# Kernel tuning notes

Measured on AMD Instinct MI355X. Metric: run time of the kernel, lower is better.

The kernel has to match this reference:

```python
import jax, jax.numpy as jnp
import numpy as np

D = 1024
H = 16
HD = D // H
DFF = 4 * D
EPS = 1e-12


def setup_inputs() -> dict:
    key = jax.random.key(0)
    ks = jax.random.split(key, 16)
    s = lambda fan_in: 1.0 / np.sqrt(fan_in)
    inp = {
        "x": jax.random.normal(ks[0], (2, 2048, D), dtype=jnp.float32),
        "Wq": jax.random.normal(ks[1], (D, D), dtype=jnp.float32) * s(D),
        "bq": jax.random.normal(ks[2], (D,), dtype=jnp.float32) * 0.02,
        "Wk": jax.random.normal(ks[3], (D, D), dtype=jnp.float32) * s(D),
        "bk": jax.random.normal(ks[4], (D,), dtype=jnp.float32) * 0.02,
        "Wv": jax.random.normal(ks[5], (D, D), dtype=jnp.float32) * s(D),
        "bv": jax.random.normal(ks[6], (D,), dtype=jnp.float32) * 0.02,
        "Wo": jax.random.normal(ks[7], (D, D), dtype=jnp.float32) * s(D),
        "bo": jax.random.normal(ks[8], (D,), dtype=jnp.float32) * 0.02,
        "W1": jax.random.normal(ks[9], (D, DFF), dtype=jnp.float32) * s(D),
        "b1": jax.random.normal(ks[10], (DFF,), dtype=jnp.float32) * 0.02,
        "W2": jax.random.normal(ks[11], (DFF, D), dtype=jnp.float32) * s(DFF),
        "b2": jax.random.normal(ks[12], (D,), dtype=jnp.float32) * 0.02,
        "g1": jnp.ones((D,), dtype=jnp.float32),
        "s1": jnp.zeros((D,), dtype=jnp.float32),
        "g2": jnp.ones((D,), dtype=jnp.float32),
        "s2": jnp.zeros((D,), dtype=jnp.float32),
    }
    return inp


def _layer_norm(x, scale, shift):
    mean = jnp.mean(x, axis=-1, keepdims=True)
    # torch.var default is unbiased (ddof=1), matching the source module
    var = jnp.var(x, axis=-1, keepdims=True, ddof=1)
    return scale * (x - mean) / jnp.sqrt(var + EPS) + shift


def _gelu(x):
    c = jnp.sqrt(jnp.asarray(2.0 / np.pi, dtype=x.dtype))
    return 0.5 * x * (1.0 + jnp.tanh(c * (x + 0.044715 * x ** 3)))


def _block(x, Wq, bq, Wk, bk, Wv, bv, Wo, bo, W1, b1, W2, b2, g1, s1, g2, s2):
    B, S, _ = x.shape
    # pre-norm attention
    h = _layer_norm(x, g1, s1)
    q = (h @ Wq + bq).reshape(B, S, H, HD).transpose(0, 2, 1, 3)  # bhsd
    k = (h @ Wk + bk).reshape(B, S, H, HD).transpose(0, 2, 1, 3)
    v = (h @ Wv + bv).reshape(B, S, H, HD).transpose(0, 2, 1, 3)
    scores = jnp.einsum("bhqd,bhkd->bhqk", q, k)
    causal = jnp.tril(jnp.ones((S, S), dtype=bool))  # True = keep
    scores = jnp.where(causal, scores, -jnp.inf)
    attn = jax.nn.softmax(scores / np.sqrt(HD), axis=-1)
    ctx = jnp.einsum("bhqk,bhkd->bhqd", attn, v)
    ctx = ctx.transpose(0, 2, 1, 3).reshape(B, S, D)
    x = x + (ctx @ Wo + bo)
    # pre-norm MLP
    h = _layer_norm(x, g2, s2)
    h = _gelu(h @ W1 + b1) @ W2 + b2
    return x + h


def reference(x, Wq, bq, Wk, bk, Wv, bv, Wo, bo, W1, b1, W2, b2, g1, s1, g2, s2):
    return _block(x, Wq, bq, Wk, bk, Wv, bv, Wo, bo, W1, b1, W2, b2, g1, s1, g2, s2)
```

## Files before the change

kernel.cpp:

```cpp
#include <hip/hip_runtime.h>

#define D_ 1024
#define H_ 16
#define HD_ 64
#define DFF_ 4096
#define B_ 2
#define S_ 2048
#define MTOK 4096

typedef unsigned short u16;
typedef short bf16x8 __attribute__((ext_vector_type(8)));
typedef float f32x4 __attribute__((ext_vector_type(4)));

__device__ __forceinline__ u16 f2bf(float f) {
    union { float f; unsigned u; } v; v.f = f;
    return (u16)((v.u + 0x7fffu + ((v.u >> 16) & 1u)) >> 16);
}
__device__ __forceinline__ u16 f2bf_ru(float f) {
    union { float f; unsigned u; } v; v.f = f;
    return (u16)((v.u + 0x8000u) >> 16);
}

__device__ __forceinline__ void gload16(const void* g, void* l) {
    __builtin_amdgcn_global_load_lds(
        (const __attribute__((address_space(1))) unsigned int*)g,
        (__attribute__((address_space(3))) unsigned int*)l, 16, 0, 0);
}

__global__ __launch_bounds__(256) void transpose_cast_kernel(
    const float* __restrict__ W, u16* __restrict__ Wt, int K, int N) {
    __shared__ float t[32][33];
    int n0 = blockIdx.x * 32, k0 = blockIdx.y * 32;
    int tx = threadIdx.x, ty = threadIdx.y;
#pragma unroll
    for (int i = 0; i < 4; i++)
        t[ty + i * 8][tx] = W[(size_t)(k0 + ty + i * 8) * N + n0 + tx];
    __syncthreads();
#pragma unroll
    for (int i = 0; i < 4; i++)
        Wt[(size_t)(n0 + ty + i * 8) * K + k0 + tx] = f2bf(t[tx][ty + i * 8]);
}

__global__ __launch_bounds__(256) void ln_kernel(
    const float* __restrict__ x, const float* __restrict__ gamma,
    const float* __restrict__ beta, u16* __restrict__ out) {
    int row = blockIdx.x, tid = threadIdx.x;
    int wave = tid >> 6, lane = tid & 63;
    const float4* xr = (const float4*)(x + (size_t)row * D_);
    float4 v = xr[tid];
    float s = v.x + v.y + v.z + v.w;
#pragma unroll
    for (int off = 1; off < 64; off <<= 1) s += __shfl_xor(s, off, 64);
    __shared__ float p1[4], p2[4];
    if (lane == 0) p1[wave] = s;
    __syncthreads();
    float mean = (p1[0] + p1[1] + p1[2] + p1[3]) * (1.0f / D_);
    float4 d = {v.x - mean, v.y - mean, v.z - mean, v.w - mean};
    float sq = d.x * d.x + d.y * d.y + d.z * d.z + d.w * d.w;
#pragma unroll
    for (int off = 1; off < 64; off <<= 1) sq += __shfl_xor(sq, off, 64);
    if (lane == 0) p2[wave] = sq;
    __syncthreads();
    float var = (p2[0] + p2[1] + p2[2] + p2[3]) * (1.0f / (D_ - 1));
    float rstd = rsqrtf(var + 1e-12f);
    float4 gv = ((const float4*)gamma)[tid];
    float4 bv = ((const float4*)beta)[tid];
    u16* orow = out + (size_t)row * D_ + tid * 4;
    orow[0] = f2bf(gv.x * d.x * rstd + bv.x);
    orow[1] = f2bf(gv.y * d.y * rstd + bv.y);
    orow[2] = f2bf(gv.z * d.z * rstd + bv.z);
    orow[3] = f2bf(gv.w * d.w * rstd + bv.w);
}

constexpr int EPI_QKV = 0, EPI_O = 3, EPI_G = 4, EPI_R = 5;

template <int EPI, int KD, int TM, int BK, int GYB>
__global__ __launch_bounds__(256) void gemm_kernel(
    const u16* __restrict__ A, const u16* __restrict__ Bt,
    const float* __restrict__ bias, const float* __restrict__ bias2,
    const float* __restrict__ bias3, const float* __restrict__ resid,
    void* __restrict__ Cout) {
    __shared__ alignas(16) char Alds[2][TM * BK * 2];
    __shared__ alignas(16) char Blds[2][128 * BK * 2];
    int tid = threadIdx.x;
    int tm = (blockIdx.x & ((1 << GYB) - 1)) * TM;
    int tn = (blockIdx.x >> GYB) * 128;
    int wave = tid >> 6, lane = tid & 63;
    int wrow = (wave >> 1) * (TM / 2), wcol = (wave & 1) * 64;
    int lcol = lane & 15, quad = lane >> 4;
    constexpr int NI = TM / 32;
    f32x4 acc[NI][4] = {};

    const u16 *ga, *gb;
    if constexpr (BK == 32) {
        int l = lane >> 3, p = lane & 7, slog = p ^ l;
        int sro = l * 2 + (slog >> 2), sch = slog & 3;
        ga = A + (size_t)(tm + wave * 16 + sro) * KD + sch * 8;
        gb = Bt + (size_t)(tn + wave * 16 + sro) * KD + sch * 8;
    } else {
        int g = (lane & 7) ^ (lane >> 3);
        ga = A + (size_t)(tm + wave * 16 + (lane >> 3)) * KD + g * 8;
        gb = Bt + (size_t)(tn + wave * 32 + (lane >> 3)) * KD + g * 8;
    }

    auto stage = [&](int k0, int buf) {
        if constexpr (BK == 32) {
            char* lA = Alds[buf] + wave * 1024;
            char* lB = Blds[buf] + wave * 1024;
            gload16(ga + k0, lA);
            if constexpr (TM == 128) gload16(ga + (size_t)64 * KD + k0, lA + 4096);
            gload16(gb + k0, lB);
            gload16(gb + (size_t)64 * KD + k0, lB + 4096);
        } else {
            char* lA = Alds[buf] + wave * 2048;
            gload16(ga + k0, lA);
            gload16(ga + (size_t)8 * KD + k0, lA + 1024);
            char* lB = Blds[buf] + wave * 4096;
            gload16(gb + k0, lB);
            gload16(gb + (size_t)8 * KD + k0, lB + 1024);
            gload16(gb + (size_t)16 * KD + k0, lB + 2048);
            gload16(gb + (size_t)24 * KD + k0, lB + 3072);
        }
    };

    constexpr int NT = KD / BK;
    stage(0, 0);
    int cur = 0;
#pragma unroll 1
    for (int kt = 0; kt < NT; kt++) {
        __syncthreads();
        if (kt + 1 < NT) stage((kt + 1) * BK, cur ^ 1);
        if constexpr (BK == 32) {
            int swz = (lcol >> 1) * 128 + (((((lcol & 1) << 2) | quad) ^ (lcol >> 1)) * 16);
            bf16x8 af[NI], bfr[4];
#pragma unroll
            for (int i = 0; i < NI; i++)
                af[i] = *(const bf16x8*)(Alds[cur] + wrow * 64 + i * 1024 + swz);
#pragma unroll
            for (int j = 0; j < 4; j++)
                bfr[j] = *(const bf16x8*)(Blds[cur] + wcol * 64 + j * 1024 + swz);
#pragma unroll
            for (int i = 0; i < NI; i++)
#pragma unroll
                for (int j = 0; j < 4; j++)
                    acc[i][j] = __builtin_amdgcn_mfma_f32_16x16x32_bf16(
                        af[i], bfr[j], acc[i][j], 0, 0, 0);
        } else {
            int koff0 = lcol * 128 + ((quad ^ (lcol & 7)) * 16);
            int koff1 = lcol * 128 + (((4 | quad) ^ (lcol & 7)) * 16);
            bf16x8 af0[NI], af1[NI], bf0[4], bf1[4];
#pragma unroll
            for (int i = 0; i < NI; i++) {
                af0[i] = *(const bf16x8*)(Alds[cur] + (wrow + i * 16) * 128 + koff0);
                af1[i] = *(const bf16x8*)(Alds[cur] + (wrow + i * 16) * 128 + koff1);
            }
#pragma unroll
            for (int j = 0; j < 4; j++) {
                bf0[j] = *(const bf16x8*)(Blds[cur] + (wcol + j * 16) * 128 + koff0);
                bf1[j] = *(const bf16x8*)(Blds[cur] + (wcol + j * 16) * 128 + koff1);
            }
#pragma unroll
            for (int i = 0; i < NI; i++)
#pragma unroll
                for (int j = 0; j < 4; j++)
                    acc[i][j] = __builtin_amdgcn_mfma_f32_16x16x32_bf16(
                        af0[i], bf0[j], acc[i][j], 0, 0, 0);
#pragma unroll
            for (int i = 0; i < NI; i++)
#pragma unroll
                for (int j = 0; j < 4; j++)
                    acc[i][j] = __builtin_amdgcn_mfma_f32_16x16x32_bf16(
                        af1[i], bf1[j], acc[i][j], 0, 0, 0);
        }
        cur ^= 1;
    }
#pragma unroll
    for (int i = 0; i < NI; i++)
#pragma unroll
        for (int j = 0; j < 4; j++)
#pragma unroll
            for (int r = 0; r < 4; r++) {
                int m = tm + wrow + i * 16 + quad * 4 + r;
                int n = tn + wcol + j * 16 + lcol;
                if constexpr (EPI == EPI_QKV) {
                    int which = n >> 10, d = n & 1023;
                    const float* bp = (which == 0) ? bias : (which == 1) ? bias2 : bias3;
                    float cval = acc[i][j][r] + bp[d];
                    int b = m >> 11, s = m & 2047, h = d >> 6, hd = d & 63;
                    u16* qkv = (u16*)Cout;
                    if (which == 0)
                        qkv[((size_t)(b * H_ + h) * S_ + s) * HD_ + hd] = f2bf(cval);
                    else if (which == 1)
                        qkv[4194304u + ((size_t)(b * H_ + h) * S_ + s) * HD_ + hd] = f2bf(cval);
                    else
                        qkv[8388608u + ((size_t)(b * H_ + h) * HD_ + hd) * S_ + s] = f2bf(cval);
                } else if constexpr (EPI == EPI_O) {
                    float cval = acc[i][j][r] + bias[n];
                    ((float*)Cout)[(size_t)m * D_ + n] = resid[(size_t)m * D_ + n] + cval;
                } else if constexpr (EPI == EPI_G) {
                    float cval = acc[i][j][r] + bias[n];
                    float u = 0.7978845608028654f * (cval + 0.044715f * cval * cval * cval);
                    float t = 1.0f - 2.0f / (__expf(2.0f * u) + 1.0f);
                    ((u16*)Cout)[(size_t)m * DFF_ + n] = f2bf(0.5f * cval * (1.0f + t));
                } else {
                    float cval = acc[i][j][r] + bias[n];
                    ((float*)Cout)[(size_t)m * D_ + n] = resid[(size_t)m * D_ + n] + cval;
                }
            }
}

__global__ __launch_bounds__(256) void attn_kernel(
    const u16* __restrict__ q, const u16* __restrict__ k,
    const u16* __restrict__ v, u16* __restrict__ ctx) {
    __shared__ alignas(16) u16 klds[2][64 * 64];
    __shared__ alignas(16) u16 vlds[2][64 * 64];
    __shared__ alignas(16) u16 plds[4][16 * 64];
    int tid = threadIdx.x, wave = tid >> 6, lane = tid & 63;
    int quad = lane >> 4, lcol = lane & 15;
    int bh = blockIdx.x & 31, pairi = blockIdx.x >> 5;
    const u16* qbase = q + (size_t)bh * S_ * HD_;
    const u16* kbase = k + (size_t)bh * S_ * HD_;
    const u16* vbase = v + (size_t)bh * HD_ * S_;
    int g = (lane & 7) ^ (lane >> 3);
    int srow = wave * 16 + (lane >> 3);
    const u16* kp = kbase + (size_t)srow * HD_ + g * 8;
    const u16* vp = vbase + (size_t)srow * S_ + g * 8;
    char* kd0 = (char*)klds[0] + wave * 2048;
    char* kd1 = (char*)klds[1] + wave * 2048;
    char* vd0 = (char*)vlds[0] + wave * 2048;
    char* vd1 = (char*)vlds[1] + wave * 2048;
    char* pbase = (char*)plds + wave * 2048;
    int koff0 = lcol * 128 + ((quad ^ (lcol & 7)) * 16);
    int koff1 = lcol * 128 + (((4 | quad) ^ (lcol & 7)) * 16);
    int b = bh >> 4, h = bh & 15;
#pragma unroll 1
    for (int half = 0; half < 2; half++) {
        int qt = half ? (31 - pairi) : pairi;
        int qr = qt * 64 + wave * 16;
        bf16x8 aq0 = *(const bf16x8*)(qbase + (size_t)(qr + lcol) * HD_ + quad * 8);
        bf16x8 aq1 = *(const bf16x8*)(qbase + (size_t)(qr + lcol) * HD_ + 32 + quad * 8);
        f32x4 co[4] = {};
        float li[4] = {0.0f, 0.0f, 0.0f, 0.0f};
        __syncthreads();
        gload16(kp, kd0);
        gload16(kp + (size_t)8 * HD_, kd0 + 1024);
        gload16(vp, vd0);
        gload16(vp + 8 * S_, vd0 + 1024);
        int cur = 0;
#pragma unroll 1
        for (int kt = 0; kt <= qt; kt++) {
            __syncthreads();
            if (kt < qt) {
                int k0 = (kt + 1) * 64;
                char* kd = cur ? kd0 : kd1;
                char* vd = cur ? vd0 : vd1;
                gload16(kp + (size_t)k0 * HD_, kd);
                gload16(kp + (size_t)(k0 + 8) * HD_, kd + 1024);
                gload16(vp + k0, vd);
                gload16(vp + 8 * S_ + k0, vd + 1024);
            }
            const u16* kl = klds[cur];
            const u16* vl = vlds[cur];
            f32x4 cs[4] = {};
#pragma unroll
            for (int j = 0; j < 4; j++) {
                bf16x8 bk = *(const bf16x8*)((char*)kl + j * 2048 + koff0);
                cs[j] = __builtin_amdgcn_mfma_f32_16x16x32_bf16(aq0, bk, cs[j], 0, 0, 0);
            }
#pragma unroll
            for (int j = 0; j < 4; j++) {
                bf16x8 bk = *(const bf16x8*)((char*)kl + j * 2048 + koff1);
                cs[j] = __builtin_amdgcn_mfma_f32_16x16x32_bf16(aq1, bk, cs[j], 0, 0, 0);
            }
            bool diag = (kt == qt);
#pragma unroll
            for (int r = 0; r < 4; r++) {
                int rr = quad * 4 + r;
                float p[4], ls = 0.0f;
#pragma unroll
                for (int j = 0; j < 4; j++) {
                    float sv = cs[j][r];
                    if (diag && (j * 16 + lcol > wave * 16 + rr)) sv = -1e38f;
                    p[j] = exp2f(sv * 0.18033688011112042f);
                    ls += p[j];
                }
                li[r] += ls;
                int pr = rr * 128 + (lcol & 7) * 2;
#pragma unroll
                for (int j = 0; j < 4; j++)
                    *(u16*)(pbase + pr + (((j * 2 + (lcol >> 3)) ^ (rr & 7)) * 16)) = f2bf_ru(p[j]);
            }
            {
                bf16x8 ap0 = *(const bf16x8*)(pbase + koff0);
                bf16x8 ap1 = *(const bf16x8*)(pbase + koff1);
#pragma unroll
                for (int j = 0; j < 4; j++) {
                    bf16x8 bv0 = *(const bf16x8*)((char*)vl + j * 2048 + koff0);
                    co[j] = __builtin_amdgcn_mfma_f32_16x16x32_bf16(ap0, bv0, co[j], 0, 0, 0);
                }
#pragma unroll
                for (int j = 0; j < 4; j++) {
                    bf16x8 bv1 = *(const bf16x8*)((char*)vl + j * 2048 + koff1);
                    co[j] = __builtin_amdgcn_mfma_f32_16x16x32_bf16(ap1, bv1, co[j], 0, 0, 0);
                }
            }
            cur ^= 1;
        }
#pragma unroll
        for (int r = 0; r < 4; r++) {
            float l = li[r];
            l += __shfl_xor(l, 1);
            l += __shfl_xor(l, 2);
            l += __shfl_xor(l, 4);
            l += __shfl_xor(l, 8);
            float inv = 1.0f / l;
            int row = qr + quad * 4 + r;
            size_t base = ((size_t)(b * S_ + row)) * D_ + h * HD_;
#pragma unroll
            for (int j = 0; j < 4; j++)
                ctx[base + j * 16 + lcol] = f2bf(co[j][r] * inv);
        }
    }
}

extern "C" void kernel_launch(void* const* d_in, const int* in_sizes, int n_in,
                              void* d_out, int out_size, void* d_ws, size_t ws_size,
                              hipStream_t stream) {
    const float* x  = (const float*)d_in[0];
    const float* Wq = (const float*)d_in[1];
    const float* bq = (const float*)d_in[2];
    const float* Wk = (const float*)d_in[3];
    const float* bk = (const float*)d_in[4];
    const float* Wv = (const float*)d_in[5];
    const float* bv = (const float*)d_in[6];
    const float* Wo = (const float*)d_in[7];
    const float* bo = (const float*)d_in[8];
    const float* W1 = (const float*)d_in[9];
    const float* b1 = (const float*)d_in[10];
    const float* W2 = (const float*)d_in[11];
    const float* b2 = (const float*)d_in[12];
    const float* g1 = (const float*)d_in[13];
    const float* s1 = (const float*)d_in[14];
    const float* g2 = (const float*)d_in[15];
    const float* s2 = (const float*)d_in[16];

    char* ws = (char*)d_ws;
    const size_t MB = 1024 * 1024;
    u16*   bWqkv = (u16*)(ws + 0 * MB);
    u16*   bWo   = (u16*)(ws + 6 * MB);
    u16*   bW1   = (u16*)(ws + 8 * MB);
    u16*   bW2   = (u16*)(ws + 16 * MB);
    u16*   hbuf  = (u16*)(ws + 24 * MB);
    u16*   qbuf  = (u16*)(ws + 32 * MB);
    u16*   ctxb  = (u16*)(ws + 56 * MB);
    float* x1    = (float*)(ws + 64 * MB);
    u16*   ffb   = (u16*)(ws + 80 * MB);

    dim3 tb(32, 8);
    transpose_cast_kernel<<<dim3(32, 32), tb, 0, stream>>>(Wq, bWqkv, D_, D_);
    transpose_cast_kernel<<<dim3(32, 32), tb, 0, stream>>>(Wk, bWqkv + 1024 * 1024, D_, D_);
    transpose_cast_kernel<<<dim3(32, 32), tb, 0, stream>>>(Wv, bWqkv + 2 * 1024 * 1024, D_, D_);
    transpose_cast_kernel<<<dim3(32, 32), tb, 0, stream>>>(Wo, bWo, D_, D_);
    transpose_cast_kernel<<<dim3(128, 32), tb, 0, stream>>>(W1, bW1, D_, DFF_);
    transpose_cast_kernel<<<dim3(32, 128), tb, 0, stream>>>(W2, bW2, DFF_, D_);

    ln_kernel<<<MTOK, 256, 0, stream>>>(x, g1, s1, hbuf);

    gemm_kernel<EPI_QKV, D_, 128, 32, 5><<<768, 256, 0, stream>>>(
        hbuf, bWqkv, bq, bk, bv, nullptr, qbuf);

    attn_kernel<<<512, 256, 0, stream>>>(
        qbuf, qbuf + 4194304u, qbuf + 8388608u, ctxb);

    gemm_kernel<EPI_O, D_, 64, 64, 6><<<512, 256, 0, stream>>>(
        ctxb, bWo, bo, nullptr, nullptr, x, x1);

    ln_kernel<<<MTOK, 256, 0, stream>>>(x1, g2, s2, hbuf);

    gemm_kernel<EPI_G, D_, 128, 32, 5><<<1024, 256, 0, stream>>>(
        hbuf, bW1, b1, nullptr, nullptr, nullptr, ffb);

    gemm_kernel<EPI_R, DFF_, 64, 64, 6><<<512, 256, 0, stream>>>(
        ffb, bW2, b2, nullptr, nullptr, x1, (float*)d_out);
}
```

Before: 357.9 us.

## Triple-buffer GEMM and attention loads and merge weight transposes into one launch

The GEMM and attention kernels move from double-buffered LDS staging with a full __syncthreads per tile to a three-slot ring that prefetches two tiles ahead. Each step waits with a partial s_waitcnt vmcnt followed by a raw s_barrier. The six weight transpose/cast launches are merged into one kernel that dispatches on block index, cutting launch overhead. The cost is 50% more LDS per block, which may lower occupancy, and the hand-set vmcnt values must match the exact number of loads issued per stage.

```diff
diff --git a/kernel.cpp b/kernel.cpp
--- a/kernel.cpp
+++ b/kernel.cpp
@@ -27,18 +27,38 @@
         (__attribute__((address_space(3))) unsigned int*)l, 16, 0, 0);
 }
 
-__global__ __launch_bounds__(256) void transpose_cast_kernel(
-    const float* __restrict__ W, u16* __restrict__ Wt, int K, int N) {
-    __shared__ float t[32][33];
-    int n0 = blockIdx.x * 32, k0 = blockIdx.y * 32;
+__global__ __launch_bounds__(256) void transpose_all_kernel(
+    const float* __restrict__ Wq, const float* __restrict__ Wk,
+    const float* __restrict__ Wv, const float* __restrict__ Wo,
+    const float* __restrict__ W1, const float* __restrict__ W2,
+    u16* __restrict__ bQKV, u16* __restrict__ bWo,
+    u16* __restrict__ bW1, u16* __restrict__ bW2) {
+    int b = blockIdx.x;
+    const float* W; u16* Wt; int K, N, nt, kt;
+    if (b < 4096) {
+        int w = b >> 10, t = b & 1023;
+        K = 1024; N = 1024; nt = t & 31; kt = t >> 5;
+        W = (w == 0) ? Wq : (w == 1) ? Wk : (w == 2) ? Wv : Wo;
+        Wt = (w < 3) ? (bQKV + (size_t)w * 1048576u) : bWo;
+    } else if (b < 8192) {
+        int t = b - 4096;
+        K = 1024; N = 4096; nt = t & 127; kt = t >> 7;
+        W = W1; Wt = bW1;
+    } else {
+        int t = b - 8192;
+        K = 4096; N = 1024; nt = t & 31; kt = t >> 5;
+        W = W2; Wt = bW2;
+    }
+    __shared__ float tl[32][33];
+    int n0 = nt * 32, k0 = kt * 32;
     int tx = threadIdx.x, ty = threadIdx.y;
 #pragma unroll
     for (int i = 0; i < 4; i++)
-        t[ty + i * 8][tx] = W[(size_t)(k0 + ty + i * 8) * N + n0 + tx];
+        tl[ty + i * 8][tx] = W[(size_t)(k0 + ty + i * 8) * N + n0 + tx];
     __syncthreads();
 #pragma unroll
     for (int i = 0; i < 4; i++)
-        Wt[(size_t)(n0 + ty + i * 8) * K + k0 + tx] = f2bf(t[tx][ty + i * 8]);
+        Wt[(size_t)(n0 + ty + i * 8) * K + k0 + tx] = f2bf(tl[tx][ty + i * 8]);
 }
 
 __global__ __launch_bounds__(256) void ln_kernel(
@@ -80,8 +100,8 @@
     const float* __restrict__ bias, const float* __restrict__ bias2,
     const float* __restrict__ bias3, const float* __restrict__ resid,
     void* __restrict__ Cout) {
-    __shared__ alignas(16) char Alds[2][TM * BK * 2];
-    __shared__ alignas(16) char Blds[2][128 * BK * 2];
+    __shared__ alignas(16) char Alds[3][TM * BK * 2];
+    __shared__ alignas(16) char Blds[3][128 * BK * 2];
     int tid = threadIdx.x;
     int tm = (blockIdx.x & ((1 << GYB) - 1)) * TM;
     int tn = (blockIdx.x >> GYB) * 128;
@@ -89,6 +109,7 @@
     int wrow = (wave >> 1) * (TM / 2), wcol = (wave & 1) * 64;
     int lcol = lane & 15, quad = lane >> 4;
     constexpr int NI = TM / 32;
+    constexpr int G = (BK == 32) ? 4 : 6;
     f32x4 acc[NI][4] = {};
 
     const u16 *ga, *gb;
@@ -103,19 +124,19 @@
         gb = Bt + (size_t)(tn + wave * 32 + (lane >> 3)) * KD + g * 8;
     }
 
-    auto stage = [&](int k0, int buf) {
+    auto stage = [&](int k0, int slot) {
         if constexpr (BK == 32) {
-            char* lA = Alds[buf] + wave * 1024;
-            char* lB = Blds[buf] + wave * 1024;
+            char* lA = Alds[slot] + wave * 1024;
+            char* lB = Blds[slot] + wave * 1024;
             gload16(ga + k0, lA);
-            if constexpr (TM == 128) gload16(ga + (size_t)64 * KD + k0, lA + 4096);
+            gload16(ga + (size_t)64 * KD + k0, lA + 4096);
             gload16(gb + k0, lB);
             gload16(gb + (size_t)64 * KD + k0, lB + 4096);
         } else {
-            char* lA = Alds[buf] + wave * 2048;
+            char* lA = Alds[slot] + wave * 2048;
             gload16(ga + k0, lA);
             gload16(ga + (size_t)8 * KD + k0, lA + 1024);
-            char* lB = Blds[buf] + wave * 4096;
+            char* lB = Blds[slot] + wave * 4096;
             gload16(gb + k0, lB);
             gload16(gb + (size_t)8 * KD + k0, lB + 1024);
             gload16(gb + (size_t)16 * KD + k0, lB + 2048);
@@ -125,11 +146,19 @@
 
     constexpr int NT = KD / BK;
     stage(0, 0);
-    int cur = 0;
+    stage(BK, 1);
 #pragma unroll 1
     for (int kt = 0; kt < NT; kt++) {
-        __syncthreads();
-        if (kt + 1 < NT) stage((kt + 1) * BK, cur ^ 1);
+        if (kt == NT - 1) {
+            asm volatile("s_waitcnt vmcnt(0)" ::: "memory");
+        } else if constexpr (G == 4) {
+            asm volatile("s_waitcnt vmcnt(4)" ::: "memory");
+        } else {
+            asm volatile("s_waitcnt vmcnt(6)" ::: "memory");
+        }
+        asm volatile("s_barrier" ::: "memory");
+        if (kt + 2 < NT) stage((kt + 2) * BK, (kt + 2) % 3);
+        int cur = kt % 3;
         if constexpr (BK == 32) {
             int swz = (lcol >> 1) * 128 + (((((lcol & 1) << 2) | quad) ^ (lcol >> 1)) * 16);
             bf16x8 af[NI], bfr[4];
@@ -172,7 +201,6 @@
                     acc[i][j] = __builtin_amdgcn_mfma_f32_16x16x32_bf16(
                         af1[i], bf1[j], acc[i][j], 0, 0, 0);
         }
-        cur ^= 1;
     }
 #pragma unroll
     for (int i = 0; i < NI; i++)
@@ -212,8 +240,8 @@
 __global__ __launch_bounds__(256) void attn_kernel(
     const u16* __restrict__ q, const u16* __restrict__ k,
     const u16* __restrict__ v, u16* __restrict__ ctx) {
-    __shared__ alignas(16) u16 klds[2][64 * 64];
-    __shared__ alignas(16) u16 vlds[2][64 * 64];
+    __shared__ alignas(16) u16 klds[3][64 * 64];
+    __shared__ alignas(16) u16 vlds[3][64 * 64];
     __shared__ alignas(16) u16 plds[4][16 * 64];
     int tid = threadIdx.x, wave = tid >> 6, lane = tid & 63;
     int quad = lane >> 4, lcol = lane & 15;
@@ -225,14 +253,19 @@
     int srow = wave * 16 + (lane >> 3);
     const u16* kp = kbase + (size_t)srow * HD_ + g * 8;
     const u16* vp = vbase + (size_t)srow * S_ + g * 8;
-    char* kd0 = (char*)klds[0] + wave * 2048;
-    char* kd1 = (char*)klds[1] + wave * 2048;
-    char* vd0 = (char*)vlds[0] + wave * 2048;
-    char* vd1 = (char*)vlds[1] + wave * 2048;
     char* pbase = (char*)plds + wave * 2048;
     int koff0 = lcol * 128 + ((quad ^ (lcol & 7)) * 16);
     int koff1 = lcol * 128 + (((4 | quad) ^ (lcol & 7)) * 16);
     int b = bh >> 4, h = bh & 15;
+    auto stage = [&](int kt, int slot) {
+        int k0 = kt * 64;
+        char* kd = (char*)klds[slot] + wave * 2048;
+        char* vd = (char*)vlds[slot] + wave * 2048;
+        gload16(kp + (size_t)k0 * HD_, kd);
+        gload16(kp + (size_t)(k0 + 8) * HD_, kd + 1024);
+        gload16(vp + k0, vd);
+        gload16(vp + 8 * S_ + k0, vd + 1024);
+    };
 #pragma unroll 1
     for (int half = 0; half < 2; half++) {
         int qt = half ? (31 - pairi) : pairi;
@@ -242,25 +275,19 @@
         f32x4 co[4] = {};
         float li[4] = {0.0f, 0.0f, 0.0f, 0.0f};
         __syncthreads();
-        gload16(kp, kd0);
-        gload16(kp + (size_t)8 * HD_, kd0 + 1024);
-        gload16(vp, vd0);
-        gload16(vp + 8 * S_, vd0 + 1024);
-        int cur = 0;
+        stage(0, 0);
+        if (qt >= 1) stage(1, 1);
 #pragma unroll 1
         for (int kt = 0; kt <= qt; kt++) {
-            __syncthreads();
-            if (kt < qt) {
-                int k0 = (kt + 1) * 64;
-                char* kd = cur ? kd0 : kd1;
-                char* vd = cur ? vd0 : vd1;
-                gload16(kp + (size_t)k0 * HD_, kd);
-                gload16(kp + (size_t)(k0 + 8) * HD_, kd + 1024);
-                gload16(vp + k0, vd);
-                gload16(vp + 8 * S_ + k0, vd + 1024);
-            }
-            const u16* kl = klds[cur];
-            const u16* vl = vlds[cur];
+            if (kt == qt) {
+                asm volatile("s_waitcnt vmcnt(0)" ::: "memory");
+            } else {
+                asm volatile("s_waitcnt vmcnt(4)" ::: "memory");
+            }
+            asm volatile("s_barrier" ::: "memory");
+            if (kt + 2 <= qt) stage(kt + 2, (kt + 2) % 3);
+            const u16* kl = klds[kt % 3];
+            const u16* vl = vlds[kt % 3];
             f32x4 cs[4] = {};
 #pragma unroll
             for (int j = 0; j < 4; j++) {
@@ -304,7 +331,6 @@
                     co[j] = __builtin_amdgcn_mfma_f32_16x16x32_bf16(ap1, bv1, co[j], 0, 0, 0);
                 }
             }
-            cur ^= 1;
         }
 #pragma unroll
         for (int r = 0; r < 4; r++) {
@@ -356,13 +382,8 @@
     float* x1    = (float*)(ws + 64 * MB);
     u16*   ffb   = (u16*)(ws + 80 * MB);
 
-    dim3 tb(32, 8);
-    transpose_cast_kernel<<<dim3(32, 32), tb, 0, stream>>>(Wq, bWqkv, D_, D_);
-    transpose_cast_kernel<<<dim3(32, 32), tb, 0, stream>>>(Wk, bWqkv + 1024 * 1024, D_, D_);
-    transpose_cast_kernel<<<dim3(32, 32), tb, 0, stream>>>(Wv, bWqkv + 2 * 1024 * 1024, D_, D_);
-    transpose_cast_kernel<<<dim3(32, 32), tb, 0, stream>>>(Wo, bWo, D_, D_);
-    transpose_cast_kernel<<<dim3(128, 32), tb, 0, stream>>>(W1, bW1, D_, DFF_);
-    transpose_cast_kernel<<<dim3(32, 128), tb, 0, stream>>>(W2, bW2, DFF_, D_);
+    transpose_all_kernel<<<12288, dim3(32, 8), 0, stream>>>(
+        Wq, Wk, Wv, Wo, W1, W2, bWqkv, bWo, bW1, bW2);
 
     ln_kernel<<<MTOK, 256, 0, stream>>>(x, g1, s1, hbuf);
 
```

After: 354.3 us. About the same (-1.0%).
